# Kernel tuning notes

Hardware: AMD Instinct MI355X
Metric: run time of the kernel (lower is better)

The kernel has to match this reference:

```python
import jax, jax.numpy as jnp
import numpy as np

KP_VARIANCE = 0.01


def make_coordinate_grid(h, w, dtype):
    # Normalized coordinates in [-1, 1], last dim is (x, y) as in monkey-net.
    x = 2.0 * (jnp.arange(w, dtype=dtype) / (w - 1)) - 1.0
    y = 2.0 * (jnp.arange(h, dtype=dtype) / (h - 1)) - 1.0
    xx = jnp.broadcast_to(x[None, :], (h, w))
    yy = jnp.broadcast_to(y[:, None], (h, w))
    return jnp.stack([xx, yy], axis=-1)  # (h, w, 2)


def grid_sample_bilinear(img, grid):
    # img: (N, C, H, W), grid: (N, Hg, Wg, 2) with xy in [-1, 1].
    # Bilinear, align_corners=True, zero padding (torch grid_sample defaults in monkey-net era).
    N, C, H, W = img.shape
    x = (grid[..., 0] + 1.0) * (W - 1) * 0.5
    y = (grid[..., 1] + 1.0) * (H - 1) * 0.5
    x0 = jnp.floor(x); y0 = jnp.floor(y)
    x1 = x0 + 1.0;     y1 = y0 + 1.0
    wx1 = x - x0; wx0 = 1.0 - wx1
    wy1 = y - y0; wy0 = 1.0 - wy1

    def gather(ix, iy):
        valid = ((ix >= 0) & (ix <= W - 1) & (iy >= 0) & (iy <= H - 1)).astype(img.dtype)
        ixc = jnp.clip(ix, 0, W - 1).astype(jnp.int32)
        iyc = jnp.clip(iy, 0, H - 1).astype(jnp.int32)
        vals = jax.vmap(lambda im, yy_, xx_: im[:, yy_, xx_])(img, iyc, ixc)  # (N, C, Hg, Wg)
        return vals * valid[:, None, :, :]

    out = (gather(x0, y0) * (wx0 * wy0)[:, None]
           + gather(x1, y0) * (wx1 * wy0)[:, None]
           + gather(x0, y1) * (wx0 * wy1)[:, None]
           + gather(x1, y1) * (wx1 * wy1)[:, None])
    return out


def setup_inputs() -> dict:
    key = jax.random.key(0)
    k1, k2, k3 = jax.random.split(key, 3)
    bs, c, dsrc, h, w = 4, 3, 1, 128, 128
    d, K = 8, 10
    source_image = jax.random.uniform(k1, (bs, c, dsrc, h, w), jnp.float32)
    kp_driving_mean = jax.random.uniform(k2, (bs, d, K, 2), jnp.float32, minval=-1.0, maxval=1.0)
    kp_source_mean = jax.random.uniform(k3, (bs, d, K, 2), jnp.float32, minval=-1.0, maxval=1.0)
    return {"source_image": source_image,
            "kp_driving_mean": kp_driving_mean,
            "kp_source_mean": kp_source_mean}


def reference(source_image, kp_driving_mean, kp_source_mean):
    bs, c, dsrc, h, w = source_image.shape
    _, d, K, _ = kp_driving_mean.shape
    grid = make_coordinate_grid(h, w, source_image.dtype)  # (h, w, 2)

    # Gaussian heatmaps around driving keypoints: (bs, d, K, h, w)
    diff2 = ((grid - kp_driving_mean[:, :, :, None, None, :]) ** 2).sum(-1)
    heat = jnp.exp(-0.5 * diff2 / KP_VARIANCE)
    heat = heat / heat.sum(axis=(-2, -1), keepdims=True)  # norm_const == 'sum'
    # add background feature map (zeros) as kp index 0
    heat = jnp.concatenate([jnp.zeros((bs, d, 1, h, w), heat.dtype), heat], axis=2)
    K1 = K + 1

    # keypoint motion difference: (bs, d, K1, 2)
    kp_diff = kp_source_mean - kp_driving_mean
    kp_diff = jnp.concatenate([jnp.zeros((bs, d, 1, 2), kp_diff.dtype), kp_diff], axis=2)
    diff_map = jnp.broadcast_to(kp_diff[:, :, :, :, None, None], (bs, d, K1, 2, h, w))

    # deformed source image per (frame, keypoint)
    app = jnp.broadcast_to(source_image[:, None, None], (bs, d, K1, c, dsrc, h, w))
    app = app.reshape(bs * d * K1, c * dsrc, h, w)
    deform = grid[None] + kp_diff.reshape(bs * d * K1, 1, 1, 2)  # (N, h, w, 2)
    deformed = grid_sample_bilinear(app, deform).reshape(bs, d, K1, c * dsrc, h, w)

    enc = jnp.concatenate([heat[:, :, :, None], diff_map, deformed], axis=3)  # (bs,d,K1,1+2+c,h,w)
    enc = enc.reshape(bs, d, -1, h, w)
    enc = jnp.transpose(enc, (0, 2, 1, 3, 4))  # (bs, out_channels, d, h, w)
    return enc
```

## Files before the change

### kernel.cpp

```cpp
#include <hip/hip_runtime.h>
#include <hip/hip_bf16.h>
#include <math.h>

#define BS 4
#define C  3
#define D  8
#define K  10
#define K1 11
#define H  128
#define W  128
#define HW (H*W)

__global__ void memb_norm_kernel(const float* __restrict__ kpd,
                                 float* __restrict__ norm) {
    int idx = blockIdx.x;
    float kx = kpd[idx * 2 + 0];
    float ky = kpd[idx * 2 + 1];
    int lane = threadIdx.x;
    float sx = 0.f, sy = 0.f;
    #pragma unroll
    for (int j = lane; j < W; j += 64) {
        float coord = (float)j * (2.0f / 127.0f) - 1.0f;
        float ddx = coord - kx;
        float ddy = coord - ky;
        sx += __expf(-50.0f * ddx * ddx);
        sy += __expf(-50.0f * ddy * ddy);
    }
    #pragma unroll
    for (int o = 32; o > 0; o >>= 1) {
        sx += __shfl_down(sx, o, 64);
        sy += __shfl_down(sy, o, 64);
    }
    if (lane == 0) norm[idx] = 1.0f / (sx * sy);
}

__global__ void memb_main_kernel(const float* __restrict__ src,
                                 const float* __restrict__ kpd,
                                 const float* __restrict__ kps,
                                 const float* __restrict__ norm,
                                 float* __restrict__ out) {
    int t = blockIdx.x * blockDim.x + threadIdx.x;
    const int total = BS * D * K1 * HW;
    if (t >= total) return;

    int wi = t & (W - 1);
    int hi = (t >> 7) & (H - 1);
    int k  = (t >> 14) % K1;
    int r  = (t >> 14) / K1;
    int di = r & (D - 1);
    int b  = r >> 3;

    float x = (float)wi * (2.0f / 127.0f) - 1.0f;
    float y = (float)hi * (2.0f / 127.0f) - 1.0f;

    float heat = 0.f, dx = 0.f, dy = 0.f;
    if (k > 0) {
        int kidx = r * K + (k - 1);
        float kx  = kpd[kidx * 2 + 0];
        float kyv = kpd[kidx * 2 + 1];
        dx = kps[kidx * 2 + 0] - kx;
        dy = kps[kidx * 2 + 1] - kyv;
        float ex = x - kx, ey = y - kyv;
        heat = __expf(-50.0f * (ex * ex + ey * ey)) * norm[kidx];
    }

    float px = (x + dx + 1.0f) * 63.5f;
    float py = (y + dy + 1.0f) * 63.5f;
    float fx0 = floorf(px), fy0 = floorf(py);
    int x0 = (int)fx0, y0 = (int)fy0;
    int x1 = x0 + 1,   y1 = y0 + 1;
    float wx1 = px - fx0, wy1 = py - fy0;
    float wx0 = 1.0f - wx1, wy0 = 1.0f - wy1;

    float vx0 = (x0 >= 0 && x0 <= W - 1) ? 1.0f : 0.0f;
    float vx1 = (x1 >= 0 && x1 <= W - 1) ? 1.0f : 0.0f;
    float vy0 = (y0 >= 0 && y0 <= H - 1) ? 1.0f : 0.0f;
    float vy1 = (y1 >= 0 && y1 <= H - 1) ? 1.0f : 0.0f;

    int cx0 = min(max(x0, 0), W - 1), cx1 = min(max(x1, 0), W - 1);
    int cy0 = min(max(y0, 0), H - 1), cy1 = min(max(y1, 0), H - 1);

    float w00 = wx0 * wy0 * vx0 * vy0;
    float w10 = wx1 * wy0 * vx1 * vy0;
    float w01 = wx0 * wy1 * vx0 * vy1;
    float w11 = wx1 * wy1 * vx1 * vy1;

    const float* sb = src + (size_t)b * C * HW;
    int o00 = cy0 * W + cx0, o10 = cy0 * W + cx1;
    int o01 = cy1 * W + cx0, o11 = cy1 * W + cx1;

    float v[C];
    #pragma unroll
    for (int ci = 0; ci < C; ci++) {
        const float* sc = sb + ci * HW;
        v[ci] = w00 * sc[o00] + w10 * sc[o10] + w01 * sc[o01] + w11 * sc[o11];
    }

    const size_t cs = (size_t)D * HW;
    size_t base = ((size_t)(b * 66 + k * 6) * D + di) * HW + hi * W + wi;
    out[base + 0 * cs] = heat;
    out[base + 1 * cs] = dx;
    out[base + 2 * cs] = dy;
    out[base + 3 * cs] = v[0];
    out[base + 4 * cs] = v[1];
    out[base + 5 * cs] = v[2];
}

extern "C" void kernel_launch(void* const* d_in, const int* in_sizes, int n_in,
                              void* d_out, int out_size, void* d_ws, size_t ws_size,
                              hipStream_t stream) {
    const float* src = (const float*)d_in[0];
    const float* kpd = (const float*)d_in[1];
    const float* kps = (const float*)d_in[2];
    float* out  = (float*)d_out;
    float* norm = (float*)d_ws;

    memb_norm_kernel<<<BS * D * K, 64, 0, stream>>>(kpd, norm);

    const int total = BS * D * K1 * HW;
    const int block = 256;
    const int grid = (total + block - 1) / block;
    memb_main_kernel<<<grid, block, 0, stream>>>(src, kpd, kps, norm, out);
}
```

Measured before the change: 157.2 us.

## Process four pixels per thread with separable heatmap and shared-shift bilinear sampling

Each thread now handles four consecutive pixels and uses a 2D grid with one y-block per (batch, frame, keypoint), so keypoint parameters are loaded once per block. The bilinear shift is constant per keypoint, which lets the sample reuse five neighbouring columns across the four outputs via vector loads. The Gaussian is split into separable x and y exponentials. Stores become float4, cutting store instruction count on this write-bound kernel, at the cost of a divergent border branch and unaligned vector loads.

```diff
diff --git a/kernel.cpp b/kernel.cpp
--- a/kernel.cpp
+++ b/kernel.cpp
@@ -1,5 +1,4 @@
 #include <hip/hip_runtime.h>
-#include <hip/hip_bf16.h>
 #include <math.h>
 
 #define BS 4
@@ -10,6 +9,8 @@
 #define H  128
 #define W  128
 #define HW (H*W)
+
+typedef float float4a __attribute__((ext_vector_type(4), aligned(4)));
 
 __global__ void memb_norm_kernel(const float* __restrict__ kpd,
                                  float* __restrict__ norm) {
@@ -39,71 +40,101 @@
                                  const float* __restrict__ kps,
                                  const float* __restrict__ norm,
                                  float* __restrict__ out) {
-    int t = blockIdx.x * blockDim.x + threadIdx.x;
-    const int total = BS * D * K1 * HW;
-    if (t >= total) return;
-
-    int wi = t & (W - 1);
-    int hi = (t >> 7) & (H - 1);
-    int k  = (t >> 14) % K1;
-    int r  = (t >> 14) / K1;
+    int rk = blockIdx.y;
+    int k  = rk % K1;
+    int r  = rk / K1;
     int di = r & (D - 1);
     int b  = r >> 3;
 
-    float x = (float)wi * (2.0f / 127.0f) - 1.0f;
-    float y = (float)hi * (2.0f / 127.0f) - 1.0f;
-
-    float heat = 0.f, dx = 0.f, dy = 0.f;
+    float kx = 0.f, ky = 0.f, dx = 0.f, dy = 0.f, nrm = 0.f;
     if (k > 0) {
         int kidx = r * K + (k - 1);
-        float kx  = kpd[kidx * 2 + 0];
-        float kyv = kpd[kidx * 2 + 1];
-        dx = kps[kidx * 2 + 0] - kx;
-        dy = kps[kidx * 2 + 1] - kyv;
-        float ex = x - kx, ey = y - kyv;
-        heat = __expf(-50.0f * (ex * ex + ey * ey)) * norm[kidx];
+        kx  = kpd[kidx * 2 + 0];
+        ky  = kpd[kidx * 2 + 1];
+        dx  = kps[kidx * 2 + 0] - kx;
+        dy  = kps[kidx * 2 + 1] - ky;
+        nrm = norm[kidx];
     }
 
-    float px = (x + dx + 1.0f) * 63.5f;
-    float py = (y + dy + 1.0f) * 63.5f;
-    float fx0 = floorf(px), fy0 = floorf(py);
-    int x0 = (int)fx0, y0 = (int)fy0;
-    int x1 = x0 + 1,   y1 = y0 + 1;
-    float wx1 = px - fx0, wy1 = py - fy0;
-    float wx0 = 1.0f - wx1, wy0 = 1.0f - wy1;
+    int p   = (blockIdx.x * blockDim.x + threadIdx.x) << 2;
+    int wi0 = p & (W - 1);
+    int hi  = p >> 7;
 
-    float vx0 = (x0 >= 0 && x0 <= W - 1) ? 1.0f : 0.0f;
-    float vx1 = (x1 >= 0 && x1 <= W - 1) ? 1.0f : 0.0f;
-    float vy0 = (y0 >= 0 && y0 <= H - 1) ? 1.0f : 0.0f;
-    float vy1 = (y1 >= 0 && y1 <= H - 1) ? 1.0f : 0.0f;
+    float y  = (float)hi * (2.0f / 127.0f) - 1.0f;
+    float ey = y - ky;
+    float expy = __expf(-50.0f * ey * ey) * nrm;
+    float heat[4];
+    #pragma unroll
+    for (int j = 0; j < 4; j++) {
+        float x  = (float)(wi0 + j) * (2.0f / 127.0f) - 1.0f;
+        float ex = x - kx;
+        heat[j] = expy * __expf(-50.0f * ex * ex);
+    }
 
-    int cx0 = min(max(x0, 0), W - 1), cx1 = min(max(x1, 0), W - 1);
-    int cy0 = min(max(y0, 0), H - 1), cy1 = min(max(y1, 0), H - 1);
+    float cx = 63.5f * dx, cy = 63.5f * dy;
+    float fsx = floorf(cx), fsy = floorf(cy);
+    float fx = cx - fsx,    fy = cy - fsy;
+    int   sx = (int)fsx,    sy = (int)fsy;
+    float wx0 = 1.0f - fx,  wx1 = fx;
 
-    float w00 = wx0 * wy0 * vx0 * vy0;
-    float w10 = wx1 * wy0 * vx1 * vy0;
-    float w01 = wx0 * wy1 * vx0 * vy1;
-    float w11 = wx1 * wy1 * vx1 * vy1;
+    int iy0 = hi + sy, iy1 = iy0 + 1;
+    float rv0 = (iy0 >= 0 && iy0 < H) ? (1.0f - fy) : 0.0f;
+    float rv1 = (iy1 >= 0 && iy1 < H) ? fy : 0.0f;
+    int cy0 = min(max(iy0, 0), H - 1);
+    int cy1 = min(max(iy1, 0), H - 1);
 
+    int c0 = wi0 + sx;
     const float* sb = src + (size_t)b * C * HW;
-    int o00 = cy0 * W + cx0, o10 = cy0 * W + cx1;
-    int o01 = cy1 * W + cx0, o11 = cy1 * W + cx1;
 
-    float v[C];
-    #pragma unroll
-    for (int ci = 0; ci < C; ci++) {
-        const float* sc = sb + ci * HW;
-        v[ci] = w00 * sc[o00] + w10 * sc[o10] + w01 * sc[o01] + w11 * sc[o11];
+    float v[C][4];
+    if (c0 >= 0 && c0 <= W - 5) {
+        #pragma unroll
+        for (int ci = 0; ci < C; ci++) {
+            const float* r0 = sb + ci * HW + cy0 * W;
+            const float* r1 = sb + ci * HW + cy1 * W;
+            float4a a  = *(const float4a*)(r0 + c0);
+            float   a4 = r0[c0 + 4];
+            float4a bq = *(const float4a*)(r1 + c0);
+            float   b4 = r1[c0 + 4];
+            float m0 = rv0 * a[0] + rv1 * bq[0];
+            float m1 = rv0 * a[1] + rv1 * bq[1];
+            float m2 = rv0 * a[2] + rv1 * bq[2];
+            float m3 = rv0 * a[3] + rv1 * bq[3];
+            float m4 = rv0 * a4   + rv1 * b4;
+            v[ci][0] = wx0 * m0 + wx1 * m1;
+            v[ci][1] = wx0 * m1 + wx1 * m2;
+            v[ci][2] = wx0 * m2 + wx1 * m3;
+            v[ci][3] = wx0 * m3 + wx1 * m4;
+        }
+    } else {
+        #pragma unroll
+        for (int ci = 0; ci < C; ci++) {
+            const float* r0 = sb + ci * HW + cy0 * W;
+            const float* r1 = sb + ci * HW + cy1 * W;
+            float m[5];
+            #pragma unroll
+            for (int i = 0; i < 5; i++) {
+                int q = c0 + i;
+                bool ok = (q >= 0) && (q < W);
+                int qc = min(max(q, 0), W - 1);
+                float mm = rv0 * r0[qc] + rv1 * r1[qc];
+                m[i] = ok ? mm : 0.0f;
+            }
+            v[ci][0] = wx0 * m[0] + wx1 * m[1];
+            v[ci][1] = wx0 * m[1] + wx1 * m[2];
+            v[ci][2] = wx0 * m[2] + wx1 * m[3];
+            v[ci][3] = wx0 * m[3] + wx1 * m[4];
+        }
     }
 
     const size_t cs = (size_t)D * HW;
-    size_t base = ((size_t)(b * 66 + k * 6) * D + di) * HW + hi * W + wi;
-    out[base + 0 * cs] = heat;
-    out[base + 1 * cs] = dx;
-    out[base + 2 * cs] = dy;
-    out[base + 3 * cs] = v[0];
-    out[base + 4 * cs] = v[1];
-    out[base + 5 * cs] = v[2];
+    size_t base = ((size_t)(b * 66 + k * 6) * D + di) * HW + (size_t)hi * W + wi0;
+    *(float4*)(out + base + 0 * cs) = make_float4(heat[0], heat[1], heat[2], heat[3]);
+    *(float4*)(out + base + 1 * cs) = make_float4(dx, dx, dx, dx);
+    *(float4*)(out + base + 2 * cs) = make_float4(dy, dy, dy, dy);
+    *(float4*)(out + base + 3 * cs) = make_float4(v[0][0], v[0][1], v[0][2], v[0][3]);
+    *(float4*)(out + base + 4 * cs) = make_float4(v[1][0], v[1][1], v[1][2], v[1][3]);
+    *(float4*)(out + base + 5 * cs) = make_float4(v[2][0], v[2][1], v[2][2], v[2][3]);
 }
 
 extern "C" void kernel_launch(void* const* d_in, const int* in_sizes, int n_in,
@@ -117,8 +148,6 @@
 
     memb_norm_kernel<<<BS * D * K, 64, 0, stream>>>(kpd, norm);
 
-    const int total = BS * D * K1 * HW;
-    const int block = 256;
-    const int grid = (total + block - 1) / block;
-    memb_main_kernel<<<grid, block, 0, stream>>>(src, kpd, kps, norm, out);
+    dim3 grid(HW / (256 * 4), BS * D * K1);
+    memb_main_kernel<<<grid, 256, 0, stream>>>(src, kpd, kps, norm, out);
 }
```

Measured after the change: 149.8 us. 4.7% less time.
